# Kernel tuning notes

Measured on AMD Instinct MI355X. Metric: run time of the kernel, lower is better.

## Reference

```python
import jax, jax.numpy as jnp
import numpy as np

N_NODES = 50000
N_EDGES = 800000
A_DIM = 128
B_DIM = 128


def setup_inputs() -> dict:
    key = jax.random.key(0)
    k1, k2, k3, k4, k5, k6 = jax.random.split(key, 6)
    edge_rows = jax.random.randint(k1, (N_EDGES,), 0, N_NODES, dtype=jnp.int32)
    edge_cols = jax.random.randint(k2, (N_EDGES,), 0, N_NODES, dtype=jnp.int32)
    edge_vals = jax.random.uniform(k3, (N_EDGES,), dtype=jnp.float32)
    H = jax.random.normal(k4, (N_NODES, A_DIM), dtype=jnp.float32)
    std = 1.0 / np.sqrt(B_DIM)
    W = jax.random.uniform(k5, (A_DIM, B_DIM), minval=-std, maxval=std, dtype=jnp.float32)
    bias = jax.random.uniform(k6, (B_DIM,), minval=-std, maxval=std, dtype=jnp.float32)
    return {"edge_rows": edge_rows, "edge_cols": edge_cols, "edge_vals": edge_vals,
            "H": H, "W": W, "bias": bias}


def reference(edge_rows, edge_cols, edge_vals, H, W, bias):
    # HW = H @ W  (dense GEMM)
    HW = jnp.matmul(H, W)  # [n, b]
    # AHW = A @ HW where A is sparse COO: A[r, c] = v
    msgs = edge_vals[:, None] * HW[edge_cols]  # [nnz, b]
    AHW = jax.ops.segment_sum(msgs, edge_rows, num_segments=H.shape[0])  # [n, b]
    return AHW + bias
```

## Files before the change

### kernel.cpp

```cpp
#include <hip/hip_runtime.h>
#include <hip/hip_fp16.h>

#define ADIM 128
#define BDIM 128
#define CAP  64
#define NT   8
#define NKS  4

typedef _Float16 half8 __attribute__((ext_vector_type(8)));
typedef float    f32x4 __attribute__((ext_vector_type(4)));
typedef unsigned int uint;
typedef unsigned short ushort;

__global__ __launch_bounds__(256) void prep_kernel(const float* __restrict__ W,
                                                   _Float16* __restrict__ Bh,
                                                   _Float16* __restrict__ Bl,
                                                   int* __restrict__ counts,
                                                   int n_nodes) {
    const int gid = blockIdx.x * 256 + threadIdx.x;
    if (blockIdx.x < 8) {
        const int l  = gid & 63;
        const int ks = (gid >> 6) & 3;
        const int t  = gid >> 8;
        const int kbase = ks * 32 + (l >> 4) * 8;
        const int col   = t * 16 + (l & 15);
        half8 hi, lo;
#pragma unroll
        for (int j = 0; j < 8; ++j) {
            const float w = W[(size_t)(kbase + j) * BDIM + col];
            const _Float16 h = (_Float16)w;
            hi[j] = h;
            lo[j] = (_Float16)(w - (float)h);
        }
        const size_t off = ((size_t)(t * NKS + ks) * 64 + l) * 8;
        *(half8*)(Bh + off) = hi;
        *(half8*)(Bl + off) = lo;
    } else {
        const int idx = gid - 2048;
        if (idx < n_nodes) counts[idx] = 0;
    }
}

__global__ __launch_bounds__(256) void gemm_kernel(
        const float* __restrict__ H,
        const _Float16* __restrict__ Bh, const _Float16* __restrict__ Bl,
        _Float16* __restrict__ HWh, int n_nodes) {
    const int tid   = threadIdx.x;
    const int l     = tid & 63;
    const int w     = tid >> 6;
    const int row_m = l & 15;
    const int kq    = l >> 4;
    const int n_strips = n_nodes >> 4;

    const int s0 = (int)blockIdx.x * 8 + w * 2;
    const bool ok0 = (s0 + 0) < n_strips;
    const bool ok1 = (s0 + 1) < n_strips;
    const int r0 = (s0 + 0) << 4;
    const int r1 = (s0 + 1) << 4;

    f32x4 acc[2][NT];
#pragma unroll
    for (int i = 0; i < 2; ++i)
#pragma unroll
        for (int t = 0; t < NT; ++t) acc[i][t] = (f32x4){0.f, 0.f, 0.f, 0.f};

#pragma unroll
    for (int ks = 0; ks < NKS; ++ks) {
        half8 ah[2], al[2];
#pragma unroll
        for (int i = 0; i < 2; ++i) {
            const bool ok = i ? ok1 : ok0;
            if (ok) {
                const int rr = (i ? r1 : r0) + row_m;
                const float4 x =
                    *(const float4*)(H + (size_t)rr * ADIM + ks * 32 + kq * 8);
                const float4 y =
                    *(const float4*)(H + (size_t)rr * ADIM + ks * 32 + kq * 8 + 4);
                const float xv[8] = {x.x, x.y, x.z, x.w, y.x, y.y, y.z, y.w};
#pragma unroll
                for (int j = 0; j < 8; ++j) {
                    const _Float16 h = (_Float16)xv[j];
                    ah[i][j] = h;
                    al[i][j] = (_Float16)(xv[j] - (float)h);
                }
            }
        }
#pragma unroll
        for (int t = 0; t < NT; ++t) {
            const size_t off = ((size_t)(t * NKS + ks) * 64 + l) * 8;
            const half8 bh = *(const half8*)(Bh + off);
            const half8 bl = *(const half8*)(Bl + off);
            if (ok0) {
                acc[0][t] = __builtin_amdgcn_mfma_f32_16x16x32_f16(ah[0], bh, acc[0][t], 0, 0, 0);
                acc[0][t] = __builtin_amdgcn_mfma_f32_16x16x32_f16(ah[0], bl, acc[0][t], 0, 0, 0);
                acc[0][t] = __builtin_amdgcn_mfma_f32_16x16x32_f16(al[0], bh, acc[0][t], 0, 0, 0);
            }
            if (ok1) {
                acc[1][t] = __builtin_amdgcn_mfma_f32_16x16x32_f16(ah[1], bh, acc[1][t], 0, 0, 0);
                acc[1][t] = __builtin_amdgcn_mfma_f32_16x16x32_f16(ah[1], bl, acc[1][t], 0, 0, 0);
                acc[1][t] = __builtin_amdgcn_mfma_f32_16x16x32_f16(al[1], bh, acc[1][t], 0, 0, 0);
            }
        }
    }

#pragma unroll
    for (int i = 0; i < 2; ++i) {
        const bool ok = i ? ok1 : ok0;
        if (!ok) continue;
        const int rb = (i ? r1 : r0) + kq * 4;
#pragma unroll
        for (int t = 0; t < NT; ++t)
#pragma unroll
            for (int r = 0; r < 4; ++r)
                HWh[(size_t)(rb + r) * BDIM + t * 16 + row_m] =
                    (_Float16)acc[i][t][r];
    }
}

__global__ __launch_bounds__(256) void bucket_kernel(const int* __restrict__ rows,
                                                     const int* __restrict__ cols,
                                                     const float* __restrict__ vals,
                                                     int* __restrict__ counts,
                                                     uint* __restrict__ ebuf,
                                                     int n_edges) {
    const int g4 = blockIdx.x * 256 + threadIdx.x;
    const int e0 = g4 * 4;
    if (e0 >= n_edges) return;

    if (e0 + 4 <= n_edges) {
        const int4   r4 = *(const int4*)(rows + e0);
        const int4   c4 = *(const int4*)(cols + e0);
        const float4 v4 = *(const float4*)(vals + e0);
        const int   rr[4] = {r4.x, r4.y, r4.z, r4.w};
        const int   cc[4] = {c4.x, c4.y, c4.z, c4.w};
        const float vv[4] = {v4.x, v4.y, v4.z, v4.w};
#pragma unroll
        for (int u = 0; u < 4; ++u) {
            const int pos = atomicAdd(&counts[rr[u]], 1);
            if (pos < CAP)
                ebuf[(size_t)rr[u] * CAP + pos] =
                    ((uint)cc[u] << 16) |
                    (uint)__half_as_ushort(__float2half(vv[u]));
        }
    } else {
        for (int e = e0; e < n_edges; ++e) {
            const int r = rows[e];
            const int pos = atomicAdd(&counts[r], 1);
            if (pos < CAP)
                ebuf[(size_t)r * CAP + pos] =
                    ((uint)cols[e] << 16) |
                    (uint)__half_as_ushort(__float2half(vals[e]));
        }
    }
}

__global__ __launch_bounds__(256) void gather_kernel(const int* __restrict__ counts,
                                                     const uint* __restrict__ ebuf,
                                                     const _Float16* __restrict__ HWh,
                                                     const float* __restrict__ bias,
                                                     float* __restrict__ out,
                                                     int n_nodes) {
    const int lane = threadIdx.x & 63;
    const int q    = lane >> 4;
    const int t    = lane & 15;
    const int node = (int)((blockIdx.x * (long)blockDim.x + threadIdx.x) >> 6);
    if (node >= n_nodes) return;

    int deg = __builtin_amdgcn_readfirstlane(counts[node]);
    if (deg > CAP) deg = CAP;

    const uint* ebn = ebuf + (size_t)node * CAP;

    float acc[8];
#pragma unroll
    for (int j = 0; j < 8; ++j) acc[j] = 0.f;

    for (int i0 = 0; i0 < deg; i0 += 16) {
        uint e[4];
#pragma unroll
        for (int u = 0; u < 4; ++u) {
            const int idx = i0 + q + 4 * u;
            e[u] = (idx < deg) ? ebn[idx] : 0u;
        }
        int4 h[4];
#pragma unroll
        for (int u = 0; u < 4; ++u)
            h[u] = *(const int4*)(HWh + (size_t)(e[u] >> 16) * BDIM + t * 8);
#pragma unroll
        for (int u = 0; u < 4; ++u) {
            __half_raw hr; hr.x = (ushort)(e[u] & 0xFFFFu);
            const float v = __half2float(*(__half*)&hr);
            const __half2* hp = (const __half2*)&h[u];
#pragma unroll
            for (int j = 0; j < 4; ++j) {
                const float2 f = __half22float2(hp[j]);
                acc[2 * j + 0] += f.x * v;
                acc[2 * j + 1] += f.y * v;
            }
        }
    }

#pragma unroll
    for (int j = 0; j < 8; ++j) {
        acc[j] += __shfl_xor(acc[j], 16, 64);
        acc[j] += __shfl_xor(acc[j], 32, 64);
    }

    if (q < 2) {
        const float4 b = ((const float4*)bias)[t * 2 + q];
        const float4 o = make_float4(acc[4 * q + 0] + b.x, acc[4 * q + 1] + b.y,
                                     acc[4 * q + 2] + b.z, acc[4 * q + 3] + b.w);
        *(float4*)(out + (size_t)node * BDIM + t * 8 + q * 4) = o;
    }
}

extern "C" void kernel_launch(void* const* d_in, const int* in_sizes, int n_in,
                              void* d_out, int out_size, void* d_ws, size_t ws_size,
                              hipStream_t stream) {
    const int*   edge_rows = (const int*)d_in[0];
    const int*   edge_cols = (const int*)d_in[1];
    const float* edge_vals = (const float*)d_in[2];
    const float* H         = (const float*)d_in[3];
    const float* W         = (const float*)d_in[4];
    const float* bias      = (const float*)d_in[5];

    const int n_edges = in_sizes[0];
    const int n_nodes = in_sizes[3] / ADIM;

    const size_t hw_bytes   = ((size_t)n_nodes * BDIM * sizeof(_Float16) + 15) & ~(size_t)15;
    const size_t cnt_bytes  = ((size_t)n_nodes * sizeof(int) + 15) & ~(size_t)15;
    const size_t ebuf_bytes = ((size_t)n_nodes * CAP * sizeof(uint) + 15) & ~(size_t)15;
    const size_t frag_bytes = (size_t)NT * NKS * 64 * 8 * sizeof(_Float16);

    char* ws = (char*)d_ws;
    _Float16* HWh  = (_Float16*)ws;  ws += hw_bytes;
    int*      cnt  = (int*)ws;       ws += cnt_bytes;
    uint*     ebuf = (uint*)ws;      ws += ebuf_bytes;
    _Float16* Bh   = (_Float16*)ws;  ws += frag_bytes;
    _Float16* Bl   = (_Float16*)ws;

    const int zero_blocks = (n_nodes + 255) / 256;
    prep_kernel<<<8 + zero_blocks, 256, 0, stream>>>(W, Bh, Bl, cnt, n_nodes);

    const int bucket_blocks = (n_edges + 1023) / 1024;
    bucket_kernel<<<bucket_blocks, 256, 0, stream>>>(edge_rows, edge_cols,
                                                     edge_vals, cnt, ebuf, n_edges);

    const int n_strips    = n_nodes >> 4;
    const int gemm_blocks = (n_strips + 7) / 8;
    gemm_kernel<<<gemm_blocks, 256, 0, stream>>>(H, Bh, Bl, HWh, n_nodes);

    gather_kernel<<<(n_nodes + 3) / 4, 256, 0, stream>>>(cnt, ebuf, HWh, bias,
                                                         (float*)d_out, n_nodes);
}
```

Before: 184.9 us.

## Fuse GEMM and edge bucketing into one launch with padded counters

Merges the GEMM and the bucketing kernels into one launch. Blocks below gemm_blocks run the GEMM, with one 16-row strip per wave instead of two, and the remaining blocks bucket one edge per thread using nontemporal loads. The per-node counters are padded to 16 ints (64 bytes) to spread atomic contention across cache lines. The aim is to overlap the compute-bound GEMM with the atomic-bound bucketing and cut one launch, at the cost of a 16x larger counter array to zero and strided counter reads in gather.

```diff
diff --git a/kernel.cpp b/kernel.cpp
--- a/kernel.cpp
+++ b/kernel.cpp
@@ -4,6 +4,7 @@
 #define ADIM 128
 #define BDIM 128
 #define CAP  64
+#define CPAD 16
 #define NT   8
 #define NKS  4
 
@@ -16,7 +17,7 @@
                                                    _Float16* __restrict__ Bh,
                                                    _Float16* __restrict__ Bl,
                                                    int* __restrict__ counts,
-                                                   int n_nodes) {
+                                                   int n_cnt) {
     const int gid = blockIdx.x * 256 + threadIdx.x;
     if (blockIdx.x < 8) {
         const int l  = gid & 63;
@@ -37,52 +38,62 @@
         *(half8*)(Bl + off) = lo;
     } else {
         const int idx = gid - 2048;
-        if (idx < n_nodes) counts[idx] = 0;
-    }
-}
-
-__global__ __launch_bounds__(256) void gemm_kernel(
+        if (idx < n_cnt) counts[idx] = 0;
+    }
+}
+
+__global__ __launch_bounds__(256) void fused_gemm_bucket(
         const float* __restrict__ H,
         const _Float16* __restrict__ Bh, const _Float16* __restrict__ Bl,
-        _Float16* __restrict__ HWh, int n_nodes) {
-    const int tid   = threadIdx.x;
+        _Float16* __restrict__ HWh, int n_nodes, int gemm_blocks,
+        const int* __restrict__ rows, const int* __restrict__ cols,
+        const float* __restrict__ vals, int* __restrict__ counts,
+        uint* __restrict__ ebuf, int n_edges) {
+    const int tid = threadIdx.x;
+
+    if ((int)blockIdx.x >= gemm_blocks) {
+        const int e = ((int)blockIdx.x - gemm_blocks) * 256 + tid;
+        if (e < n_edges) {
+            const int   r = __builtin_nontemporal_load(rows + e);
+            const int   c = __builtin_nontemporal_load(cols + e);
+            const float v = __builtin_nontemporal_load(vals + e);
+            const int pos = atomicAdd(&counts[(size_t)r * CPAD], 1);
+            if (pos < CAP)
+                ebuf[(size_t)r * CAP + pos] =
+                    ((uint)c << 16) | (uint)__half_as_ushort(__float2half(v));
+        }
+        return;
+    }
+
     const int l     = tid & 63;
     const int w     = tid >> 6;
     const int row_m = l & 15;
     const int kq    = l >> 4;
     const int n_strips = n_nodes >> 4;
 
-    const int s0 = (int)blockIdx.x * 8 + w * 2;
-    const bool ok0 = (s0 + 0) < n_strips;
-    const bool ok1 = (s0 + 1) < n_strips;
-    const int r0 = (s0 + 0) << 4;
-    const int r1 = (s0 + 1) << 4;
-
-    f32x4 acc[2][NT];
-#pragma unroll
-    for (int i = 0; i < 2; ++i)
-#pragma unroll
-        for (int t = 0; t < NT; ++t) acc[i][t] = (f32x4){0.f, 0.f, 0.f, 0.f};
+    const int s = (int)blockIdx.x * 4 + w;
+    if (s >= n_strips) return;
+    const int r0 = s << 4;
+
+    f32x4 acc[NT];
+#pragma unroll
+    for (int t = 0; t < NT; ++t) acc[t] = (f32x4){0.f, 0.f, 0.f, 0.f};
 
 #pragma unroll
     for (int ks = 0; ks < NKS; ++ks) {
-        half8 ah[2], al[2];
-#pragma unroll
-        for (int i = 0; i < 2; ++i) {
-            const bool ok = i ? ok1 : ok0;
-            if (ok) {
-                const int rr = (i ? r1 : r0) + row_m;
-                const float4 x =
-                    *(const float4*)(H + (size_t)rr * ADIM + ks * 32 + kq * 8);
-                const float4 y =
-                    *(const float4*)(H + (size_t)rr * ADIM + ks * 32 + kq * 8 + 4);
-                const float xv[8] = {x.x, x.y, x.z, x.w, y.x, y.y, y.z, y.w};
-#pragma unroll
-                for (int j = 0; j < 8; ++j) {
-                    const _Float16 h = (_Float16)xv[j];
-                    ah[i][j] = h;
-                    al[i][j] = (_Float16)(xv[j] - (float)h);
-                }
+        half8 ah, al;
+        {
+            const int rr = r0 + row_m;
+            const float4 x =
+                *(const float4*)(H + (size_t)rr * ADIM + ks * 32 + kq * 8);
+            const float4 y =
+                *(const float4*)(H + (size_t)rr * ADIM + ks * 32 + kq * 8 + 4);
+            const float xv[8] = {x.x, x.y, x.z, x.w, y.x, y.y, y.z, y.w};
+#pragma unroll
+            for (int j = 0; j < 8; ++j) {
+                const _Float16 h = (_Float16)xv[j];
+                ah[j] = h;
+                al[j] = (_Float16)(xv[j] - (float)h);
             }
         }
 #pragma unroll
@@ -90,68 +101,18 @@
             const size_t off = ((size_t)(t * NKS + ks) * 64 + l) * 8;
             const half8 bh = *(const half8*)(Bh + off);
             const half8 bl = *(const half8*)(Bl + off);
-            if (ok0) {
-                acc[0][t] = __builtin_amdgcn_mfma_f32_16x16x32_f16(ah[0], bh, acc[0][t], 0, 0, 0);
-                acc[0][t] = __builtin_amdgcn_mfma_f32_16x16x32_f16(ah[0], bl, acc[0][t], 0, 0, 0);
-                acc[0][t] = __builtin_amdgcn_mfma_f32_16x16x32_f16(al[0], bh, acc[0][t], 0, 0, 0);
-            }
-            if (ok1) {
-                acc[1][t] = __builtin_amdgcn_mfma_f32_16x16x32_f16(ah[1], bh, acc[1][t], 0, 0, 0);
-                acc[1][t] = __builtin_amdgcn_mfma_f32_16x16x32_f16(ah[1], bl, acc[1][t], 0, 0, 0);
-                acc[1][t] = __builtin_amdgcn_mfma_f32_16x16x32_f16(al[1], bh, acc[1][t], 0, 0, 0);
-            }
-        }
-    }
-
-#pragma unroll
-    for (int i = 0; i < 2; ++i) {
-        const bool ok = i ? ok1 : ok0;
-        if (!ok) continue;
-        const int rb = (i ? r1 : r0) + kq * 4;
-#pragma unroll
-        for (int t = 0; t < NT; ++t)
-#pragma unroll
-            for (int r = 0; r < 4; ++r)
-                HWh[(size_t)(rb + r) * BDIM + t * 16 + row_m] =
-                    (_Float16)acc[i][t][r];
-    }
-}
-
-__global__ __launch_bounds__(256) void bucket_kernel(const int* __restrict__ rows,
-                                                     const int* __restrict__ cols,
-                                                     const float* __restrict__ vals,
-                                                     int* __restrict__ counts,
-                                                     uint* __restrict__ ebuf,
-                                                     int n_edges) {
-    const int g4 = blockIdx.x * 256 + threadIdx.x;
-    const int e0 = g4 * 4;
-    if (e0 >= n_edges) return;
-
-    if (e0 + 4 <= n_edges) {
-        const int4   r4 = *(const int4*)(rows + e0);
-        const int4   c4 = *(const int4*)(cols + e0);
-        const float4 v4 = *(const float4*)(vals + e0);
-        const int   rr[4] = {r4.x, r4.y, r4.z, r4.w};
-        const int   cc[4] = {c4.x, c4.y, c4.z, c4.w};
-        const float vv[4] = {v4.x, v4.y, v4.z, v4.w};
-#pragma unroll
-        for (int u = 0; u < 4; ++u) {
-            const int pos = atomicAdd(&counts[rr[u]], 1);
-            if (pos < CAP)
-                ebuf[(size_t)rr[u] * CAP + pos] =
-                    ((uint)cc[u] << 16) |
-                    (uint)__half_as_ushort(__float2half(vv[u]));
-        }
-    } else {
-        for (int e = e0; e < n_edges; ++e) {
-            const int r = rows[e];
-            const int pos = atomicAdd(&counts[r], 1);
-            if (pos < CAP)
-                ebuf[(size_t)r * CAP + pos] =
-                    ((uint)cols[e] << 16) |
-                    (uint)__half_as_ushort(__float2half(vals[e]));
-        }
-    }
+            acc[t] = __builtin_amdgcn_mfma_f32_16x16x32_f16(ah, bh, acc[t], 0, 0, 0);
+            acc[t] = __builtin_amdgcn_mfma_f32_16x16x32_f16(ah, bl, acc[t], 0, 0, 0);
+            acc[t] = __builtin_amdgcn_mfma_f32_16x16x32_f16(al, bh, acc[t], 0, 0, 0);
+        }
+    }
+
+    const int rb = r0 + kq * 4;
+#pragma unroll
+    for (int t = 0; t < NT; ++t)
+#pragma unroll
+        for (int r = 0; r < 4; ++r)
+            HWh[(size_t)(rb + r) * BDIM + t * 16 + row_m] = (_Float16)acc[t][r];
 }
 
 __global__ __launch_bounds__(256) void gather_kernel(const int* __restrict__ counts,
@@ -166,7 +127,7 @@
     const int node = (int)((blockIdx.x * (long)blockDim.x + threadIdx.x) >> 6);
     if (node >= n_nodes) return;
 
-    int deg = __builtin_amdgcn_readfirstlane(counts[node]);
+    int deg = __builtin_amdgcn_readfirstlane(counts[(size_t)node * CPAD]);
     if (deg > CAP) deg = CAP;
 
     const uint* ebn = ebuf + (size_t)node * CAP;
@@ -226,9 +187,10 @@
 
     const int n_edges = in_sizes[0];
     const int n_nodes = in_sizes[3] / ADIM;
+    const int n_cnt   = n_nodes * CPAD;
 
     const size_t hw_bytes   = ((size_t)n_nodes * BDIM * sizeof(_Float16) + 15) & ~(size_t)15;
-    const size_t cnt_bytes  = ((size_t)n_nodes * sizeof(int) + 15) & ~(size_t)15;
+    const size_t cnt_bytes  = ((size_t)n_cnt * sizeof(int) + 15) & ~(size_t)15;
     const size_t ebuf_bytes = ((size_t)n_nodes * CAP * sizeof(uint) + 15) & ~(size_t)15;
     const size_t frag_bytes = (size_t)NT * NKS * 64 * 8 * sizeof(_Float16);
 
@@ -239,16 +201,15 @@
     _Float16* Bh   = (_Float16*)ws;  ws += frag_bytes;
     _Float16* Bl   = (_Float16*)ws;
 
-    const int zero_blocks = (n_nodes + 255) / 256;
-    prep_kernel<<<8 + zero_blocks, 256, 0, stream>>>(W, Bh, Bl, cnt, n_nodes);
-
-    const int bucket_blocks = (n_edges + 1023) / 1024;
-    bucket_kernel<<<bucket_blocks, 256, 0, stream>>>(edge_rows, edge_cols,
-                                                     edge_vals, cnt, ebuf, n_edges);
-
-    const int n_strips    = n_nodes >> 4;
-    const int gemm_blocks = (n_strips + 7) / 8;
-    gemm_kernel<<<gemm_blocks, 256, 0, stream>>>(H, Bh, Bl, HWh, n_nodes);
+    const int zero_blocks = (n_cnt + 255) / 256;
+    prep_kernel<<<8 + zero_blocks, 256, 0, stream>>>(W, Bh, Bl, cnt, n_cnt);
+
+    const int n_strips      = n_nodes >> 4;
+    const int gemm_blocks   = (n_strips + 3) / 4;
+    const int bucket_blocks = (n_edges + 255) / 256;
+    fused_gemm_bucket<<<gemm_blocks + bucket_blocks, 256, 0, stream>>>(
+        H, Bh, Bl, HWh, n_nodes, gemm_blocks,
+        edge_rows, edge_cols, edge_vals, cnt, ebuf, n_edges);
 
     gather_kernel<<<(n_nodes + 3) / 4, 256, 0, stream>>>(cnt, ebuf, HWh, bias,
                                                          (float*)d_out, n_nodes);
```

New measurement: 163.5 us. 1.13x faster.
